# Performance work log

Measured on AMD Instinct MI355X. Metric: run time of the kernel, lower is better.

Reference implementation:

```python
import jax, jax.numpy as jnp
import numpy as np

# Straight-through sign binarization (Binarize in BNN code mutates .data, so
# autograd sees identity -> custom_vjp with identity backward).
@jax.custom_vjp
def binarize(x):
    return jnp.sign(x)

def _bin_fwd(x):
    return jnp.sign(x), None

def _bin_bwd(_, g):
    return (g,)

binarize.defvjp(_bin_fwd, _bin_bwd)

EPS = 1e-5  # torch BatchNorm1d default eps

def batchnorm(x, g, b):
    # training-mode BN: batch statistics, biased variance
    if x.ndim == 3:  # (N, C, L): stats over N and L
        m = x.mean(axis=(0, 2), keepdims=True)
        v = x.var(axis=(0, 2), keepdims=True)
        return (x - m) / jnp.sqrt(v + EPS) * g[None, :, None] + b[None, :, None]
    m = x.mean(axis=0)
    v = x.var(axis=0)
    return (x - m) / jnp.sqrt(v + EPS) * g + b

def hardtanh(x):
    return jnp.clip(x, -1.0, 1.0)

def maxpool3(x):
    # MaxPool1d(kernel=3, stride=3): trim then reshape-max
    N, C, L = x.shape
    Lp = L // 3
    return x[:, :, :Lp * 3].reshape(N, C, Lp, 3).max(axis=-1)

def bconv(x, w, b, binarize_input=True):
    # BinarizeConv1d: kernel 41, dilation 2, VALID padding; weights sign-binarized,
    # inputs binarized except when in_channels == 3 (first layer rule in BNN code).
    xb = binarize(x) if binarize_input else x
    wb = binarize(w)
    y = jax.lax.conv_general_dilated(
        xb, wb, window_strides=(1,), padding='VALID',
        rhs_dilation=(2,), dimension_numbers=('NCH', 'OIH', 'NCH'))
    return y + b[None, :, None]

def blinear(x, w, b):
    # BinarizeLinear: in_features 832/1024 != 784 -> binarize input and weight
    return binarize(x) @ binarize(w).T + b

def _forward(x, bn0_g, bn0_b, conv1_w, conv1_b, bn1_g, bn1_b,
             conv2_w, conv2_b, bn2_g, bn2_b, conv3_w, conv3_b,
             bn3_g, bn3_b, conv4_w, conv4_b, bn4_g, bn4_b,
             conv5_w, conv5_b, fc1_w, fc1_b, bn5_g, bn5_b,
             fc2_w, fc2_b, bn6_g, bn6_b):
    h = hardtanh(batchnorm(x, bn0_g, bn0_b))
    h = maxpool3(bconv(h, conv1_w, conv1_b, binarize_input=False))  # (N,64,5306)
    h = hardtanh(batchnorm(h, bn1_g, bn1_b))
    h = maxpool3(bconv(h, conv2_w, conv2_b))  # (N,64,1742)
    h = hardtanh(batchnorm(h, bn2_g, bn2_b))
    h = maxpool3(bconv(h, conv3_w, conv3_b))  # (N,64,554)
    h = hardtanh(batchnorm(h, bn3_g, bn3_b))
    h = maxpool3(bconv(h, conv4_w, conv4_b))  # (N,64,158)
    h = hardtanh(batchnorm(h, bn4_g, bn4_b))
    h = maxpool3(bconv(h, conv5_w, conv5_b))  # (N,32,26)
    h = h.reshape(-1, 16 * 52)                # (N, 832)
    h = hardtanh(batchnorm(blinear(h, fc1_w, fc1_b), bn5_g, bn5_b))
    h = batchnorm(blinear(h, fc2_w, fc2_b), bn6_g, bn6_b)
    return jax.nn.log_softmax(h, axis=1)

def setup_inputs() -> dict:
    key = jax.random.key(0)
    ks = jax.random.split(key, 32)
    def rn(k, shape, s=0.1):
        return jax.random.normal(k, shape, dtype=jnp.float32) * s
    def bn_params(kg, kb, c):
        return 1.0 + rn(kg, (c,)), rn(kb, (c,))
    N, L, K = 64, 16000, 41
    d = {"x": jax.random.normal(ks[0], (N, 3, L), dtype=jnp.float32)}
    d["bn0_g"], d["bn0_b"] = bn_params(ks[1], ks[2], 3)
    d["conv1_w"], d["conv1_b"] = rn(ks[3], (64, 3, K)), rn(ks[4], (64,), 0.01)
    d["bn1_g"], d["bn1_b"] = bn_params(ks[5], ks[6], 64)
    d["conv2_w"], d["conv2_b"] = rn(ks[7], (64, 64, K)), rn(ks[8], (64,), 0.01)
    d["bn2_g"], d["bn2_b"] = bn_params(ks[9], ks[10], 64)
    d["conv3_w"], d["conv3_b"] = rn(ks[11], (64, 64, K)), rn(ks[12], (64,), 0.01)
    d["bn3_g"], d["bn3_b"] = bn_params(ks[13], ks[14], 64)
    d["conv4_w"], d["conv4_b"] = rn(ks[15], (64, 64, K)), rn(ks[16], (64,), 0.01)
    d["bn4_g"], d["bn4_b"] = bn_params(ks[17], ks[18], 64)
    d["conv5_w"], d["conv5_b"] = rn(ks[19], (32, 64, K)), rn(ks[20], (32,), 0.01)
    d["fc1_w"], d["fc1_b"] = rn(ks[21], (1024, 832)), rn(ks[22], (1024,), 0.01)
    d["bn5_g"], d["bn5_b"] = bn_params(ks[23], ks[24], 1024)
    d["fc2_w"], d["fc2_b"] = rn(ks[25], (1000, 1024)), rn(ks[26], (1000,), 0.01)
    d["bn6_g"], d["bn6_b"] = bn_params(ks[27], ks[28], 1000)
    return d

def reference(x, bn0_g, bn0_b, conv1_w, conv1_b, bn1_g, bn1_b,
              conv2_w, conv2_b, bn2_g, bn2_b, conv3_w, conv3_b,
              bn3_g, bn3_b, conv4_w, conv4_b, bn4_g, bn4_b,
              conv5_w, conv5_b, fc1_w, fc1_b, bn5_g, bn5_b,
              fc2_w, fc2_b, bn6_g, bn6_b):
    return _forward(x, bn0_g, bn0_b, conv1_w, conv1_b, bn1_g, bn1_b,
                    conv2_w, conv2_b, bn2_g, bn2_b, conv3_w, conv3_b,
                    bn3_g, bn3_b, conv4_w, conv4_b, bn4_g, bn4_b,
                    conv5_w, conv5_b, fc1_w, fc1_b, bn5_g, bn5_b,
                    fc2_w, fc2_b, bn6_g, bn6_b)
```

## Files before the change

kernel.cpp:

```cpp
#include <hip/hip_runtime.h>
#include <hip/hip_bf16.h>
#include <stdint.h>

typedef __hip_bfloat16 bf16;
typedef unsigned long long u64;
typedef unsigned short u16;

typedef __attribute__((ext_vector_type(8))) short bf16x8;
typedef __attribute__((ext_vector_type(4))) float f32x4;

#define FIXCAP (1u << 20)

static __device__ __forceinline__ float ldin(const void* p, long i, int f32) {
    return f32 ? ((const float*)p)[i] : __bfloat162float(((const bf16*)p)[i]);
}

__global__ void k_probe(const void* x, unsigned* ctl) {
    int tid = threadIdx.x;
    int good = 0;
    for (int i = tid; i < 1024; i += 256) {
        float v = __bfloat162float(((const bf16*)x)[2 * i]);
        float a = fabsf(v);
        if (v == 0.0f || (isfinite(v) && a >= 1e-4f && a <= 100.0f)) good++;
    }
    __shared__ int s[256];
    s[tid] = good; __syncthreads();
    for (int st = 128; st > 0; st >>= 1) {
        if (tid < st) s[tid] += s[tid + st];
        __syncthreads();
    }
    if (tid == 0) { ctl[0] = 0u; ctl[1] = (s[0] >= 700) ? 0u : 1u; }
}

__global__ void k_sentinel(void* outv, const unsigned* ctl, float val) {
    int i = blockIdx.x * 256 + threadIdx.x;
    if (i >= 64000) return;
    if (ctl[1]) ((float*)outv)[i] = val;
    else ((bf16*)outv)[i] = __float2bfloat16(val);
}

__device__ __forceinline__ void pack_convw_task(const void* w, uint2* wp, int Co, int f32,
                                                int bx, int tid) {
    int t = bx * 256 + tid;
    if (t >= Co * 41) return;
    int co = t / 41, k = t % 41;
    unsigned w0 = 0, w1 = 0;
    for (int c = 0; c < 32; c++)
        if (ldin(w, (co * 64 + c) * 41 + k, f32) > 0.f) w0 |= (1u << c);
    for (int c = 0; c < 32; c++)
        if (ldin(w, (co * 64 + 32 + c) * 41 + k, f32) > 0.f) w1 |= (1u << c);
    wp[t] = make_uint2(w0, w1);
}
__device__ __forceinline__ void pack_rows_task(const void* w, unsigned* wp, int rows, int F,
                                               int f32, int bx, int tid) {
    int Fw = F >> 5;
    int t = bx * 256 + tid;
    if (t >= rows * Fw) return;
    int r = t / Fw, wi = t % Fw;
    unsigned m = 0;
    for (int j = 0; j < 32; j++)
        if (ldin(w, (long)r * F + wi * 32 + j, f32) > 0.f) m |= (1u << j);
    wp[t] = m;
}

__global__ void k_prep(const void* x, const void* c1w, const void* c2w, const void* c3w,
                       const void* c4w, const void* c5w, const void* f1w, const void* f2w,
                       u16* afrag, uint2* w2p, uint2* w3p, uint2* w4p, uint2* w5p,
                       unsigned* fc1wp, unsigned* fc2wp, u64* stats, double* part0,
                       const unsigned* ctl) {
    int f32 = ctl[1];
    int task = blockIdx.y, bx = blockIdx.x, tid = threadIdx.x;
    switch (task) {
        case 0: {
            int t = bx * 256 + tid;
            if (t < 2304) {
                int m = t / 576, rem = t - m * 576;
                int ks = rem / 64, lane = rem - ks * 64;
                int li = lane & 15, hq = lane >> 4;
                int row = 16 * m + li;
                int g = 4 * ks + hq;
                int c = g / 11, t0 = 4 * (g - 11 * c);
                u16* outp = afrag + (size_t)t * 8;
                for (int i2 = 0; i2 < 4; i2++) {
                    int tt = t0 + i2;
                    u16 sv = 0;
                    if (g < 33 && tt <= 40) {
                        float wv = ldin(c1w, (row * 3 + c) * 41 + tt, f32);
                        sv = (wv > 0.f) ? (u16)0x3F80 : ((wv < 0.f) ? (u16)0xBF80 : (u16)0);
                    }
                    outp[2 * i2] = sv;
                    outp[2 * i2 + 1] = sv;
                }
            }
        } break;
        case 1: pack_convw_task(c2w, w2p, 64, f32, bx, tid); break;
        case 2: pack_convw_task(c3w, w3p, 64, f32, bx, tid); break;
        case 3: pack_convw_task(c4w, w4p, 64, f32, bx, tid); break;
        case 4: pack_convw_task(c5w, w5p, 32, f32, bx, tid); break;
        case 5: pack_rows_task(f1w, fc1wp, 1024, 832, f32, bx, tid); break;
        case 6: pack_rows_task(f2w, fc2wp, 1000, 1024, f32, bx, tid); break;
        case 7: {
            int i = bx * 256 + tid;
            if (i < 14400) stats[i] = 0ull;
        } break;
        case 8: {
            if (bx >= 96) return;
            int c = bx >> 5, s = bx & 31;
            double s1 = 0, s2 = 0;
            for (int n = 0; n < 64; n++) {
                long base = (long)(n * 3 + c) * 16000;
                for (int l = s * 256 + tid; l < 16000; l += 32 * 256) {
                    double v = (double)ldin(x, base + l, f32);
                    s1 += v; s2 += v * v;
                }
            }
            __shared__ double a1[256], a2[256];
            a1[tid] = s1; a2[tid] = s2;
            __syncthreads();
            for (int st = 128; st > 0; st >>= 1) {
                if (tid < st) { a1[tid] += a1[tid + st]; a2[tid] += a2[tid + st]; }
                __syncthreads();
            }
            if (tid == 0) { part0[(c * 32 + s) * 2] = a1[0]; part0[(c * 32 + s) * 2 + 1] = a2[0]; }
        } break;
    }
}

__global__ __launch_bounds__(256, 4) void k_conv1(const void* __restrict__ x,
                                                  const double* __restrict__ part0,
                                                  const void* __restrict__ g0,
                                                  const void* __restrict__ b0,
                                                  const u16* __restrict__ afrag,
                                                  double* __restrict__ yb,
                                                  const void* __restrict__ g1,
                                                  const void* __restrict__ b1,
                                                  uint2* __restrict__ x2p,
                                                  unsigned* __restrict__ fixcnt,
                                                  unsigned* __restrict__ fixlist,
                                                  const unsigned* __restrict__ ctl,
                                                  int pass) {
    __shared__ unsigned xs[8][140];
    __shared__ float pool[4][48][20];
    __shared__ double sbuf[4][64][2];
    __shared__ unsigned char sb[4][16][64];
    __shared__ double2 pqs[64];
    __shared__ float2 b0f[3];
    int f32 = ctl[1];
    int n = blockIdx.y, bx = blockIdx.x, tid = threadIdx.x;
    if (tid < 3) {
        int c = tid;
        double s1 = 0, s2 = 0;
        for (int s = 0; s < 32; s++) { s1 += part0[(c * 32 + s) * 2]; s2 += part0[(c * 32 + s) * 2 + 1]; }
        double M = 64.0 * 16000.0;
        double mu = s1 / M, var = s2 / M - mu * mu;
        double A = (double)ldin(g0, c, f32) / sqrt(var + 1e-5);
        b0f[c] = make_float2((float)A, (float)((double)ldin(b0, c, f32) - mu * A));
    }
    if (pass && tid >= 64 && tid < 128) {
        int c = tid - 64;
        double s1 = 0, s2 = 0;
        for (int s = 0; s < 16; s++) { s1 += yb[(c * 16 + s) * 2]; s2 += yb[(c * 16 + s) * 2 + 1]; }
        double M = 64.0 * 5306.0;
        double mu = s1 / M, var = s2 / M - mu * mu;
        double A = (double)ldin(g1, c, f32) / sqrt(var + 1e-5);
        pqs[c] = make_double2(A, (double)ldin(b1, c, f32) - mu * A);
    }
    __syncthreads();

    unsigned* xsf = &xs[0][0];
    for (int f = tid; f < 1120; f += 256) {
        int rc = f / 140, qi = f - rc * 140;
        int r = rc >> 2, c = rc & 3;
        unsigned dw = 0u;
        if (c < 3) {
            int xpos = 192 * bx + 2 * qi + r;
            if (xpos < 16000) {
                float2 pb = b0f[c];
                float v = fmaf(ldin(x, (long)(n * 3 + c) * 16000 + xpos, f32), pb.x, pb.y);
                v = fminf(fmaxf(v, -1.f), 1.f);
                bf16 h = __float2bfloat16(v);
                float hf = __bfloat162float(h);
                bf16 lo = __float2bfloat16(v - hf);
                dw = (unsigned)__bfloat16_as_ushort(h) | ((unsigned)__bfloat16_as_ushort(lo) << 16);
            }
        }
        xsf[f] = dw;
    }
    __syncthreads();

    int lane = tid & 63;
    int li = lane & 15, hq = lane >> 4;
    int w = __builtin_amdgcn_readfirstlane(tid >> 6);

    f32x4 zz = {0.f, 0.f, 0.f, 0.f};
    f32x4 acc[4][3];
#pragma unroll
    for (int m = 0; m < 4; m++)
#pragma unroll
        for (int nf = 0; nf < 3; nf++) acc[m][nf] = zz;

    int boff[3];
#pragma unroll
    for (int nf = 0; nf < 3; nf++) {
        int pl = 48 * w + 16 * nf + li;
        boff[nf] = (pl & 1) * 560 + (pl >> 1);
    }

    const bf16x8* ag = (const bf16x8*)afrag;
#pragma unroll 1
    for (int ks = 0; ks < 9; ks++) {
        int g = 4 * ks + hq;
        int c = g / 11;
        int kb = c * 140 + 4 * (g - 11 * c);
        bf16x8 a0 = ag[(0 * 9 + ks) * 64 + lane];
        bf16x8 a1 = ag[(1 * 9 + ks) * 64 + lane];
        bf16x8 a2 = ag[(2 * 9 + ks) * 64 + lane];
        bf16x8 a3 = ag[(3 * 9 + ks) * 64 + lane];
#pragma unroll
        for (int nf = 0; nf < 3; nf++) {
            const unsigned* bp = xsf + boff[nf] + kb;
            union { int4 i4; bf16x8 v; } u;
            u.i4 = make_int4(bp[0], bp[1], bp[2], bp[3]);
            acc[0][nf] = __builtin_amdgcn_mfma_f32_16x16x32_bf16(a0, u.v, acc[0][nf], 0, 0, 0);
            acc[1][nf] = __builtin_amdgcn_mfma_f32_16x16x32_bf16(a1, u.v, acc[1][nf], 0, 0, 0);
            acc[2][nf] = __builtin_amdgcn_mfma_f32_16x16x32_bf16(a2, u.v, acc[2][nf], 0, 0, 0);
            acc[3][nf] = __builtin_amdgcn_mfma_f32_16x16x32_bf16(a3, u.v, acc[3][nf], 0, 0, 0);
        }
    }

    int lp0 = 64 * bx + 16 * w;
    if (pass == 0) {
#pragma unroll 1
        for (int m = 0; m < 4; m++) {
#pragma unroll
            for (int nf = 0; nf < 3; nf++)
                *(f32x4*)&pool[w][16 * nf + li][4 * hq] = acc[m][nf];
            double s = 0.0, q = 0.0;
#pragma unroll
            for (int i = 0; i < 4; i++) {
                int pc = hq + 4 * i;
                float mq = fmaxf(fmaxf(pool[w][3 * pc][li], pool[w][3 * pc + 1][li]),
                                 pool[w][3 * pc + 2][li]);
                if (lp0 + pc < 5306) {
                    double d = (double)mq;
                    s += d; q += d * d;
                }
            }
            s += __shfl_down(s, 32, 64); s += __shfl_down(s, 16, 64);
            q += __shfl_down(q, 32, 64); q += __shfl_down(q, 16, 64);
            if (lane < 16) { sbuf[w][16 * m + lane][0] = s; sbuf[w][16 * m + lane][1] = q; }
        }
        __syncthreads();
        if (tid < 64) {
            double s = sbuf[0][tid][0] + sbuf[1][tid][0] + sbuf[2][tid][0] + sbuf[3][tid][0];
            double q = sbuf[0][tid][1] + sbuf[1][tid][1] + sbuf[2][tid][1] + sbuf[3][tid][1];
            int sbk = bx & 15;
            atomicAdd(&yb[(tid * 16 + sbk) * 2], s);
            atomicAdd(&yb[(tid * 16 + sbk) * 2 + 1], q);
        }
    } else {
#pragma unroll 1
        for (int m = 0; m < 4; m++) {
#pragma unroll
            for (int nf = 0; nf < 3; nf++)
                *(f32x4*)&pool[w][16 * nf + li][4 * hq] = acc[m][nf];
            int c = 16 * m + li;
            double2 P = pqs[c];
            double athr = 2e-3 * fabs(P.x);
#pragma unroll
            for (int i = 0; i < 4; i++) {
                int pc = hq + 4 * i;
                int lp = lp0 + pc;
                float mq = fmaxf(fmaxf(pool[w][3 * pc][li], pool[w][3 * pc + 1][li]),
                                 pool[w][3 * pc + 2][li]);
                if (lp < 5306) {
                    double v = (double)mq * P.x + P.y;
                    sb[w][pc][c] = (v > 0.0) ? 1 : 0;
                    if (fabs(v) < athr) {
                        unsigned idx = atomicAdd(fixcnt, 1u);
                        if (idx < FIXCAP)
                            fixlist[idx] = ((unsigned)n << 19) | ((unsigned)c << 13) | (unsigned)lp;
                    }
                }
            }
        }
        __syncthreads();
        if (tid < 64) {
            int lp = 64 * bx + tid;
            if (lp < 5306) {
                const unsigned* sp = (const unsigned*)&sb[tid >> 4][tid & 15][0];
                unsigned w0 = 0, w1 = 0;
#pragma unroll
                for (int jw = 0; jw < 8; jw++)
                    w0 |= (((sp[jw] * 0x01020408u) >> 24) & 0xFu) << (4 * jw);
#pragma unroll
                for (int jw = 8; jw < 16; jw++)
                    w1 |= (((sp[jw] * 0x01020408u) >> 24) & 0xFu) << (4 * (jw - 8));
                x2p[(size_t)n * 5306 + lp] = make_uint2(w0, w1);
            }
        }
    }
}

__global__ void k_fix(const unsigned* __restrict__ fixcnt, const unsigned* __restrict__ fixlist,
                      const double* __restrict__ yb, const void* g1, const void* b1,
                      const void* __restrict__ x, const void* __restrict__ c1w,
                      const double* __restrict__ part0, const void* g0, const void* b0,
                      unsigned* __restrict__ x2p, const unsigned* __restrict__ ctl) {
    int f32 = ctl[1];
    unsigned cnt = min(*fixcnt, FIXCAP);
    for (unsigned t = blockIdx.x * 256 + threadIdx.x; t < cnt; t += gridDim.x * 256) {
        unsigned e = fixlist[t];
        int n = e >> 19, c = (e >> 13) & 63, l = e & 8191;
        double s1 = 0, s2 = 0;
        for (int s = 0; s < 16; s++) { s1 += yb[(c * 16 + s) * 2]; s2 += yb[(c * 16 + s) * 2 + 1]; }
        double M = 64.0 * 5306.0;
        double mu = s1 / M, var = s2 / M - mu * mu;
        double A = (double)ldin(g1, c, f32) / sqrt(var + 1e-5);
        double B = (double)ldin(b1, c, f32) - mu * A;
        double best = -1e300;
        for (int r = 0; r < 3; r++) {
            int pp = 3 * l + r;
            double acc = 0.0;
            for (int cc = 0; cc < 3; cc++) {
                double p1 = 0, p2 = 0;
                for (int s = 0; s < 32; s++) { p1 += part0[(cc * 32 + s) * 2]; p2 += part0[(cc * 32 + s) * 2 + 1]; }
                double M0 = 64.0 * 16000.0;
                double mu0 = p1 / M0, var0 = p2 / M0 - mu0 * mu0;
                double A0 = (double)ldin(g0, cc, f32) / sqrt(var0 + 1e-5);
                double B0 = (double)ldin(b0, cc, f32) - mu0 * A0;
                for (int k = 0; k < 41; k++) {
                    float wf = ldin(c1w, (c * 3 + cc) * 41 + k, f32);
                    double sgn = (wf > 0.f) ? 1.0 : ((wf < 0.f) ? -1.0 : 0.0);
                    double xv = (double)ldin(x, (long)(n * 3 + cc) * 16000 + pp + 2 * k, f32);
                    xv = fmin(fmax(xv * A0 + B0, -1.0), 1.0);
                    acc = fma(sgn, xv, acc);
                }
            }
            best = fmax(best, acc);
        }
        double v = best * A + B;
        unsigned* word = &x2p[((size_t)n * 5306 + l) * 2 + (c >> 5)];
        unsigned bit = 1u << (c & 31);
        if (v > 0.0) atomicOr(word, bit);
        else atomicAnd(word, ~bit);
    }
}

__global__ __launch_bounds__(256) void k_conv_bin(const uint2* __restrict__ xp,
                                                  const uint2* __restrict__ wp,
                                                  u16* __restrict__ mout,
                                                  int Lp, int Lin, int Co,
                                                  u64* __restrict__ stat) {
    int n = blockIdx.y, tid = threadIdx.x;
    int lane = tid & 63;
    int wave = __builtin_amdgcn_readfirstlane(tid >> 6);
    int co0 = blockIdx.z * 32 + wave * 8;
    int base = blockIdx.x * 192;
    int lp = blockIdx.x * 64 + lane;

    __shared__ uint2 xt[272];
    for (int i = tid; i < 272; i += 256) {
        int pos = base + i;
        xt[i] = (pos < Lin) ? xp[(size_t)n * Lin + pos] : make_uint2(0u, 0u);
    }
    __syncthreads();

    int acc[8][3] = {};
    uint2 xa = xt[3 * lane];
    for (int k = 0; k < 41; k++) {
        uint2 xb = xt[3 * lane + 2 * k + 1];
        uint2 xc = xt[3 * lane + 2 * k + 2];
#pragma unroll
        for (int j = 0; j < 8; j++) {
            uint2 w = wp[(co0 + j) * 41 + k];
            acc[j][0] += __popc(w.x ^ xa.x) + __popc(w.y ^ xa.y);
            acc[j][1] += __popc(w.x ^ xb.x) + __popc(w.y ^ xb.y);
            acc[j][2] += __popc(w.x ^ xc.x) + __popc(w.y ^ xc.y);
        }
        xa = xc;
    }
    bool ok = lp < Lp;
    int sb = blockIdx.x & 15;
#pragma unroll
    for (int j = 0; j < 8; j++) {
        int m = min(min(acc[j][0], acc[j][1]), acc[j][2]);
        if (ok) mout[((size_t)n * Co + co0 + j) * Lp + lp] = (u16)m;
        unsigned s = ok ? (unsigned)m : 0u;
        unsigned q = ok ? (unsigned)(m * m) : 0u;
        for (int off = 32; off > 0; off >>= 1) {
            s += __shfl_down(s, off, 64);
            q += __shfl_down(q, off, 64);
        }
        if (lane == 0) {
            atomicAdd(&stat[((co0 + j) * 16 + sb) * 2], (u64)s);
            atomicAdd(&stat[((co0 + j) * 16 + sb) * 2 + 1], (u64)q);
        }
    }
}

__global__ __launch_bounds__(256) void k_conv_binm(const u16* __restrict__ min_,
                                                   const u64* __restrict__ statIn,
                                                   const void* g, const void* b, double M,
                                                   const uint2* __restrict__ wp,
                                                   u16* __restrict__ mout,
                                                   u64* __restrict__ statOut,
                                                   int Lp, int Lin, int Co,
                                                   const unsigned* __restrict__ ctl) {
    __shared__ double2 pqs[64];
    __shared__ uint2 xt[272];
    int f32 = ctl[1];
    int n = blockIdx.y, tid = threadIdx.x;
    if (tid < 64) {
        int c = tid;
        u64 s1 = 0, s2 = 0;
        for (int s = 0; s < 16; s++) { s1 += statIn[(c * 16 + s) * 2]; s2 += statIn[(c * 16 + s) * 2 + 1]; }
        double mu = (double)s1 / M;
        double varm = (double)s2 / M - mu * mu;
        double A = (double)ldin(g, c, f32) / sqrt(4.0 * varm + 1e-5);
        pqs[c] = make_double2(-2.0 * A, 2.0 * A * mu + (double)ldin(b, c, f32));
    }
    __syncthreads();
    int base = blockIdx.x * 192;
    for (int i = tid; i < 272; i += 256) {
        int pos = base + i;
        unsigned w0 = 0, w1 = 0;
        if (pos < Lin) {
            const u16* mp = min_ + (size_t)n * 64 * Lin + pos;
#pragma unroll 4
            for (int c = 0; c < 32; c++) {
                double2 p = pqs[c];
                if ((double)mp[(size_t)c * Lin] * p.x + p.y > 0.0) w0 |= 1u << c;
            }
#pragma unroll 4
            for (int c = 0; c < 32; c++) {
                double2 p = pqs[c + 32];
                if ((double)mp[(size_t)(c + 32) * Lin] * p.x + p.y > 0.0) w1 |= 1u << c;
            }
        }
        xt[i] = make_uint2(w0, w1);
    }
    __syncthreads();

    int lane = tid & 63;
    int wave = __builtin_amdgcn_readfirstlane(tid >> 6);
    int co0 = blockIdx.z * 32 + wave * 8;
    int lp = blockIdx.x * 64 + lane;

    int acc[8][3] = {};
    uint2 xa = xt[3 * lane];
    for (int k = 0; k < 41; k++) {
        uint2 xb = xt[3 * lane + 2 * k + 1];
        uint2 xc = xt[3 * lane + 2 * k + 2];
#pragma unroll
        for (int j = 0; j < 8; j++) {
            uint2 w = wp[(co0 + j) * 41 + k];
            acc[j][0] += __popc(w.x ^ xa.x) + __popc(w.y ^ xa.y);
            acc[j][1] += __popc(w.x ^ xb.x) + __popc(w.y ^ xb.y);
            acc[j][2] += __popc(w.x ^ xc.x) + __popc(w.y ^ xc.y);
        }
        xa = xc;
    }
    bool ok = lp < Lp;
    int sb = blockIdx.x & 15;
#pragma unroll
    for (int j = 0; j < 8; j++) {
        int m = min(min(acc[j][0], acc[j][1]), acc[j][2]);
        if (ok) mout[((size_t)n * Co + co0 + j) * Lp + lp] = (u16)m;
        if (statOut) {
            unsigned s = ok ? (unsigned)m : 0u;
            unsigned q = ok ? (unsigned)(m * m) : 0u;
            for (int off = 32; off > 0; off >>= 1) {
                s += __shfl_down(s, off, 64);
                q += __shfl_down(q, off, 64);
            }
            if (lane == 0) {
                atomicAdd(&statOut[((co0 + j) * 16 + sb) * 2], (u64)s);
                atomicAdd(&statOut[((co0 + j) * 16 + sb) * 2 + 1], (u64)q);
            }
        }
    }
}

__global__ void k_c5fc1(const u16* __restrict__ m4, const u64* __restrict__ s4,
                        const void* g4, const void* b4,
                        const uint2* __restrict__ w5p, const void* __restrict__ b5,
                        const unsigned* __restrict__ fc1wp, u16* __restrict__ acc1,
                        u64* __restrict__ s5, const unsigned* __restrict__ ctl) {
    __shared__ double2 pqs[64];
    __shared__ uint2 xt[280];
    __shared__ int m5s[32][26];
    __shared__ unsigned xw[26];
    int f32 = ctl[1];
    int n = blockIdx.x, tid = threadIdx.x;
    const int Lin = 158;
    if (tid < 64) {
        int c = tid;
        u64 s1 = 0, s2 = 0;
        for (int s = 0; s < 16; s++) { s1 += s4[(c * 16 + s) * 2]; s2 += s4[(c * 16 + s) * 2 + 1]; }
        double M = 64.0 * 158.0;
        double mu = (double)s1 / M;
        double varm = (double)s2 / M - mu * mu;
        double A = (double)ldin(g4, c, f32) / sqrt(4.0 * varm + 1e-5);
        pqs[c] = make_double2(-2.0 * A, 2.0 * A * mu + (double)ldin(b4, c, f32));
    }
    __syncthreads();
    for (int i = tid; i < 280; i += 256) {
        unsigned w0 = 0, w1 = 0;
        if (i < Lin) {
            const u16* mp = m4 + (size_t)n * 64 * Lin + i;
#pragma unroll 4
            for (int c = 0; c < 32; c++) {
                double2 p = pqs[c];
                if ((double)mp[(size_t)c * Lin] * p.x + p.y > 0.0) w0 |= 1u << c;
            }
#pragma unroll 4
            for (int c = 0; c < 32; c++) {
                double2 p = pqs[c + 32];
                if ((double)mp[(size_t)(c + 32) * Lin] * p.x + p.y > 0.0) w1 |= 1u << c;
            }
        }
        xt[i] = make_uint2(w0, w1);
    }
    __syncthreads();

    int lane = tid & 63;
    int wave = __builtin_amdgcn_readfirstlane(tid >> 6);
    int co0 = wave * 8;
    int acc[8][3] = {};
    uint2 xa = xt[3 * lane];
    for (int k = 0; k < 41; k++) {
        uint2 xb = xt[3 * lane + 2 * k + 1];
        uint2 xc = xt[3 * lane + 2 * k + 2];
#pragma unroll
        for (int j = 0; j < 8; j++) {
            uint2 w = w5p[(co0 + j) * 41 + k];
            acc[j][0] += __popc(w.x ^ xa.x) + __popc(w.y ^ xa.y);
            acc[j][1] += __popc(w.x ^ xb.x) + __popc(w.y ^ xb.y);
            acc[j][2] += __popc(w.x ^ xc.x) + __popc(w.y ^ xc.y);
        }
        xa = xc;
    }
    if (lane < 26) {
#pragma unroll
        for (int j = 0; j < 8; j++)
            m5s[co0 + j][lane] = min(min(acc[j][0], acc[j][1]), acc[j][2]);
    }
    __syncthreads();
    if (tid < 26) {
        unsigned mask = 0;
        for (int j = 0; j < 32; j++) {
            int f = tid * 32 + j, c = f / 26, l = f % 26;
            double yv = 2624.0 - 2.0 * (double)m5s[c][l] + (double)ldin(b5, c, f32);
            if (yv > 0.0) mask |= 1u << j;
        }
        xw[tid] = mask;
    }
    __syncthreads();
#pragma unroll
    for (int i = 0; i < 4; i++) {
        int j = tid + i * 256;
        unsigned a = 0;
        for (int w = 0; w < 26; w++) a += __popc(xw[w] ^ fc1wp[j * 26 + w]);
        acc1[n * 1024 + j] = (u16)a;
        atomicAdd(&s5[j * 2], (u64)a);
        atomicAdd(&s5[j * 2 + 1], (u64)(a * a));
    }
}

__global__ void k_fc2(const u16* __restrict__ acc1, const u64* __restrict__ s5,
                      const void* g5, const void* b5, const unsigned* __restrict__ fc2wp,
                      u16* __restrict__ acc2, u64* __restrict__ s6, const unsigned* ctl) {
    __shared__ double2 pq5s[1024];
    __shared__ unsigned xw[32];
    int f32 = ctl[1];
    int n = blockIdx.y, tid = threadIdx.x;
    for (int f = tid; f < 1024; f += 256) {
        u64 a1 = s5[f * 2], a2 = s5[f * 2 + 1];
        double mu = (double)a1 / 64.0;
        double varm = (double)a2 / 64.0 - mu * mu;
        double A = (double)ldin(g5, f, f32) / sqrt(4.0 * varm + 1e-5);
        pq5s[f] = make_double2(-2.0 * A, 2.0 * A * mu + (double)ldin(b5, f, f32));
    }
    __syncthreads();
    if (tid < 32) {
        unsigned mask = 0;
        for (int j = 0; j < 32; j++) {
            int f = tid * 32 + j;
            double2 p = pq5s[f];
            if ((double)acc1[n * 1024 + f] * p.x + p.y > 0.0) mask |= 1u << j;
        }
        xw[tid] = mask;
    }
    __syncthreads();
    int j = blockIdx.x * 256 + tid;
    if (j >= 1000) return;
    unsigned a = 0;
    for (int w = 0; w < 32; w++) a += __popc(xw[w] ^ fc2wp[j * 32 + w]);
    acc2[n * 1000 + j] = (u16)a;
    atomicAdd(&s6[j * 2], (u64)a);
    atomicAdd(&s6[j * 2 + 1], (u64)(a * a));
}

__global__ void k_lsm(const u16* __restrict__ acc2, const u64* __restrict__ s6,
                      const void* g6, const void* b6, const unsigned* ctl, void* outv) {
    int n = blockIdx.x, tid = threadIdx.x;
    int f32 = ctl[1];
    __shared__ double red[256];
    double v[4];
    double mx = -1e300;
#pragma unroll
    for (int i = 0; i < 4; i++) {
        int j = tid + i * 256;
        if (j < 1000) {
            u64 a1 = s6[j * 2], a2 = s6[j * 2 + 1];
            double mu = (double)a1 / 64.0;
            double varm = (double)a2 / 64.0 - mu * mu;
            double A = (double)ldin(g6, j, f32) / sqrt(4.0 * varm + 1e-5);
            v[i] = (double)acc2[n * 1000 + j] * (-2.0 * A) + (2.0 * A * mu + (double)ldin(b6, j, f32));
            mx = fmax(mx, v[i]);
        } else v[i] = -1e300;
    }
    red[tid] = mx; __syncthreads();
    for (int s = 128; s > 0; s >>= 1) {
        if (tid < s) red[tid] = fmax(red[tid], red[tid + s]);
        __syncthreads();
    }
    mx = red[0]; __syncthreads();
    double sum = 0.0;
#pragma unroll
    for (int i = 0; i < 4; i++) {
        int j = tid + i * 256;
        if (j < 1000) sum += exp(v[i] - mx);
    }
    red[tid] = sum; __syncthreads();
    for (int s = 128; s > 0; s >>= 1) {
        if (tid < s) red[tid] += red[tid + s];
        __syncthreads();
    }
    double ls = log(red[0]);
#pragma unroll
    for (int i = 0; i < 4; i++) {
        int j = tid + i * 256;
        if (j < 1000) {
            float r = (float)(v[i] - mx - ls);
            if (!isfinite(r)) r = -700.0f;
            if (f32) ((float*)outv)[n * 1000 + j] = r;
            else ((bf16*)outv)[n * 1000 + j] = __float2bfloat16(r);
        }
    }
}

extern "C" void kernel_launch(void* const* d_in, const int* in_sizes, int n_in,
                              void* d_out, int out_size, void* d_ws, size_t ws_size,
                              hipStream_t stream) {
    const void* x       = d_in[0];
    const void* bn0_g   = d_in[1];
    const void* bn0_b   = d_in[2];
    const void* conv1_w = d_in[3];
    const void* bn1_g   = d_in[5];
    const void* bn1_b   = d_in[6];
    const void* conv2_w = d_in[7];
    const void* bn2_g   = d_in[9];
    const void* bn2_b   = d_in[10];
    const void* conv3_w = d_in[11];
    const void* bn3_g   = d_in[13];
    const void* bn3_b   = d_in[14];
    const void* conv4_w = d_in[15];
    const void* bn4_g   = d_in[17];
    const void* bn4_b   = d_in[18];
    const void* conv5_w = d_in[19];
    const void* conv5_b = d_in[20];
    const void* fc1_w   = d_in[21];
    const void* bn5_g   = d_in[23];
    const void* bn5_b   = d_in[24];
    const void* fc2_w   = d_in[25];
    const void* bn6_g   = d_in[27];
    const void* bn6_b   = d_in[28];

    char* wsb = (char*)d_ws;
    size_t off = 0;
    auto alloc = [&](size_t bytes) -> void* {
        off = (off + 255) & ~(size_t)255;
        void* p = wsb + off;
        off += bytes;
        return p;
    };

    unsigned* ctl   = (unsigned*)alloc(256);
    unsigned* x2p   = (unsigned*)alloc(2716672);
    u16*      m2    = (u16*)alloc(14270464);
    u16*      m3    = (u16*)alloc(4538368);
    u16*      m4    = (u16*)alloc(1294336);
    u16*      acc1  = (u16*)alloc(131072);
    u16*      acc2  = (u16*)alloc(128000);
    u16*      afrag = (u16*)alloc(36864);
    uint2*    w2p   = (uint2*)alloc(20992);
    uint2*    w3p   = (uint2*)alloc(20992);
    uint2*    w4p   = (uint2*)alloc(20992);
    uint2*    w5p   = (uint2*)alloc(10496);
    unsigned* fc1wp = (unsigned*)alloc(106496);
    unsigned* fc2wp = (unsigned*)alloc(128000);
    u64*      stats = (u64*)alloc(14400 * 8);
    double*   part0 = (double*)alloc(2048);
    unsigned* fixlist = (unsigned*)alloc(FIXCAP * 4);
    size_t need = (off + 255) & ~(size_t)255;

    u64* s2 = stats;
    u64* s3 = stats + 2048;
    u64* s4 = stats + 4096;
    u64* s5 = stats + 6144;
    u64* s6 = stats + 8192;
    double* yb = (double*)(stats + 12288);
    unsigned* fixcnt = (unsigned*)(stats + 14340);

    k_probe<<<1, 256, 0, stream>>>(x, ctl);

    if (n_in != 29) {
        k_sentinel<<<250, 256, 0, stream>>>(d_out, ctl, -(3000.0f + (float)n_in));
        return;
    }
    if (ws_size < need) {
        k_sentinel<<<250, 256, 0, stream>>>(d_out, ctl, -1500.0f);
        return;
    }

    k_prep<<<dim3(125, 9), 256, 0, stream>>>(x, conv1_w, conv2_w, conv3_w, conv4_w, conv5_w,
                                             fc1_w, fc2_w, afrag, w2p, w3p, w4p, w5p,
                                             fc1wp, fc2wp, stats, part0, ctl);

    k_conv1<<<dim3(83, 64), 256, 0, stream>>>(x, part0, bn0_g, bn0_b, afrag, yb,
                                              bn1_g, bn1_b, (uint2*)x2p,
                                              fixcnt, fixlist, ctl, 0);
    k_conv1<<<dim3(83, 64), 256, 0, stream>>>(x, part0, bn0_g, bn0_b, afrag, yb,
                                              bn1_g, bn1_b, (uint2*)x2p,
                                              fixcnt, fixlist, ctl, 1);
    k_fix<<<64, 256, 0, stream>>>(fixcnt, fixlist, yb, bn1_g, bn1_b, x, conv1_w,
                                  part0, bn0_g, bn0_b, x2p, ctl);

    k_conv_bin<<<dim3(28, 64, 2), 256, 0, stream>>>((const uint2*)x2p, w2p, m2, 1742, 5306, 64, s2);
    k_conv_binm<<<dim3(9, 64, 2), 256, 0, stream>>>(m2, s2, bn2_g, bn2_b, 64.0 * 1742.0,
                                                    w3p, m3, s3, 554, 1742, 64, ctl);
    k_conv_binm<<<dim3(3, 64, 2), 256, 0, stream>>>(m3, s3, bn3_g, bn3_b, 64.0 * 554.0,
                                                    w4p, m4, s4, 158, 554, 64, ctl);

    k_c5fc1<<<64, 256, 0, stream>>>(m4, s4, bn4_g, bn4_b, w5p, conv5_b, fc1wp, acc1, s5, ctl);
    k_fc2<<<dim3(4, 64), 256, 0, stream>>>(acc1, s5, bn5_g, bn5_b, fc2wp, acc2, s6, ctl);
    k_lsm<<<64, 256, 0, stream>>>(acc2, s6, bn6_g, bn6_b, ctl, d_out);
}
```

Measured before the change: 806.4 us.

## Replace popcount conv2 with int8 MFMA convolution over ±1 expanded bits

Conv2 (64→64 channels, binarized) was computed with XOR-popcount on packed bits. It now expands the packed input bits to ±1 int8 in LDS and pre-packs weights as ±1 int8 MFMA fragments. The convolution then runs on mfma_i32_16x16x64_i8 matrix instructions, with weight chunks streamed via global_load_lds. Pooling and stats are done through an LDS staging buffer, and the dot product is converted back to the mismatch count. The aim is to move the heavy popcount ALU work onto matrix cores, at the cost of more LDS traffic and an 8x larger input footprint.

Measured after the change: 883.1 us. +9.5%, slower.

```diff
diff --git a/kernel.cpp b/kernel.cpp
--- a/kernel.cpp
+++ b/kernel.cpp
@@ -8,6 +8,7 @@
 
 typedef __attribute__((ext_vector_type(8))) short bf16x8;
 typedef __attribute__((ext_vector_type(4))) float f32x4;
+typedef __attribute__((ext_vector_type(4))) int i32x4;
 
 #define FIXCAP (1u << 20)
 
@@ -65,7 +66,7 @@
 
 __global__ void k_prep(const void* x, const void* c1w, const void* c2w, const void* c3w,
                        const void* c4w, const void* c5w, const void* f1w, const void* f2w,
-                       u16* afrag, uint2* w2p, uint2* w3p, uint2* w4p, uint2* w5p,
+                       u16* afrag, signed char* af2, uint2* w3p, uint2* w4p, uint2* w5p,
                        unsigned* fc1wp, unsigned* fc2wp, u64* stats, double* part0,
                        const unsigned* ctl) {
     int f32 = ctl[1];
@@ -93,7 +94,31 @@
                 }
             }
         } break;
-        case 1: pack_convw_task(c2w, w2p, 64, f32, bx, tid); break;
+        case 1: {
+            int t = bx * 256 + tid;
+            if (t < 11264) {
+                int lane = t & 63, g = t >> 6;
+                int m = g & 3, tt = g >> 2;
+                int li = lane & 15, hq = lane >> 4;
+                int co = 16 * m + li;
+                unsigned dws[4];
+#pragma unroll
+                for (int dw = 0; dw < 4; dw++) {
+                    unsigned v = 0;
+                    if (tt <= 40) {
+#pragma unroll
+                        for (int b = 0; b < 4; b++) {
+                            int c = 16 * hq + 4 * dw + b;
+                            float wv = ldin(c2w, (co * 64 + c) * 41 + tt, f32);
+                            unsigned byte = (wv > 0.f) ? 0x01u : 0xFFu;
+                            v |= byte << (8 * b);
+                        }
+                    }
+                    dws[dw] = v;
+                }
+                ((uint4*)af2)[t] = make_uint4(dws[0], dws[1], dws[2], dws[3]);
+            }
+        } break;
         case 2: pack_convw_task(c3w, w3p, 64, f32, bx, tid); break;
         case 3: pack_convw_task(c4w, w4p, 64, f32, bx, tid); break;
         case 4: pack_convw_task(c5w, w5p, 32, f32, bx, tid); break;
@@ -347,54 +372,113 @@
     }
 }
 
-__global__ __launch_bounds__(256) void k_conv_bin(const uint2* __restrict__ xp,
-                                                  const uint2* __restrict__ wp,
-                                                  u16* __restrict__ mout,
-                                                  int Lp, int Lin, int Co,
-                                                  u64* __restrict__ stat) {
-    int n = blockIdx.y, tid = threadIdx.x;
+__global__ __launch_bounds__(256, 3) void k_conv_i8(const uint2* __restrict__ xp,
+                                                    const signed char* __restrict__ af2,
+                                                    u16* __restrict__ mout,
+                                                    u64* __restrict__ stat) {
+    __shared__ unsigned xsd[2 * 136 * 16];
+    __shared__ __align__(16) signed char abuf[16384];
+    __shared__ int pooli[4][48][20];
+    int n = blockIdx.y, bx = blockIdx.x, tid = threadIdx.x;
+    int base = 192 * bx;
+
+    for (int e = tid; e < 272; e += 256) {
+        int pos = base + e;
+        int r = e & 1, qi = e >> 1;
+        unsigned* dst = xsd + (r * 136 + qi) * 16;
+        if (pos < 5306) {
+            uint2 mk = xp[(size_t)n * 5306 + pos];
+#pragma unroll
+            for (int dw = 0; dw < 8; dw++) {
+                unsigned nib = (mk.x >> (4 * dw)) & 0xFu;
+                unsigned sp = (nib * 0x00204081u) & 0x01010101u;
+                dst[dw] = ~(sp * 0xFEu);
+            }
+#pragma unroll
+            for (int dw = 0; dw < 8; dw++) {
+                unsigned nib = (mk.y >> (4 * dw)) & 0xFu;
+                unsigned sp = (nib * 0x00204081u) & 0x01010101u;
+                dst[8 + dw] = ~(sp * 0xFEu);
+            }
+        } else {
+#pragma unroll
+            for (int dw = 0; dw < 16; dw++) dst[dw] = 0u;
+        }
+    }
+
     int lane = tid & 63;
-    int wave = __builtin_amdgcn_readfirstlane(tid >> 6);
-    int co0 = blockIdx.z * 32 + wave * 8;
-    int base = blockIdx.x * 192;
-    int lp = blockIdx.x * 64 + lane;
-
-    __shared__ uint2 xt[272];
-    for (int i = tid; i < 272; i += 256) {
-        int pos = base + i;
-        xt[i] = (pos < Lin) ? xp[(size_t)n * Lin + pos] : make_uint2(0u, 0u);
-    }
-    __syncthreads();
-
-    int acc[8][3] = {};
-    uint2 xa = xt[3 * lane];
-    for (int k = 0; k < 41; k++) {
-        uint2 xb = xt[3 * lane + 2 * k + 1];
-        uint2 xc = xt[3 * lane + 2 * k + 2];
-#pragma unroll
-        for (int j = 0; j < 8; j++) {
-            uint2 w = wp[(co0 + j) * 41 + k];
-            acc[j][0] += __popc(w.x ^ xa.x) + __popc(w.y ^ xa.y);
-            acc[j][1] += __popc(w.x ^ xb.x) + __popc(w.y ^ xb.y);
-            acc[j][2] += __popc(w.x ^ xc.x) + __popc(w.y ^ xc.y);
-        }
-        xa = xc;
-    }
-    bool ok = lp < Lp;
-    int sb = blockIdx.x & 15;
-#pragma unroll
-    for (int j = 0; j < 8; j++) {
-        int m = min(min(acc[j][0], acc[j][1]), acc[j][2]);
-        if (ok) mout[((size_t)n * Co + co0 + j) * Lp + lp] = (u16)m;
-        unsigned s = ok ? (unsigned)m : 0u;
-        unsigned q = ok ? (unsigned)(m * m) : 0u;
-        for (int off = 32; off > 0; off >>= 1) {
-            s += __shfl_down(s, off, 64);
-            q += __shfl_down(q, off, 64);
-        }
-        if (lane == 0) {
-            atomicAdd(&stat[((co0 + j) * 16 + sb) * 2], (u64)s);
-            atomicAdd(&stat[((co0 + j) * 16 + sb) * 2 + 1], (u64)q);
+    int li = lane & 15, hq = lane >> 4;
+    int w = __builtin_amdgcn_readfirstlane(tid >> 6);
+
+    i32x4 zz = {0, 0, 0, 0};
+    i32x4 acc[4][3];
+#pragma unroll
+    for (int m = 0; m < 4; m++)
+#pragma unroll
+        for (int nf = 0; nf < 3; nf++) acc[m][nf] = zz;
+
+    int boff[3];
+#pragma unroll
+    for (int nf = 0; nf < 3; nf++) {
+        int pl = 48 * w + 16 * nf + li;
+        boff[nf] = ((pl & 1) * 136 + (pl >> 1)) * 64 + 16 * hq;
+    }
+
+    const char* gA = (const char*)af2 + w * 4096 + lane * 16;
+    const char* xsb = (const char*)xsd;
+
+#pragma unroll 1
+    for (int ch = 0; ch < 11; ch++) {
+        __syncthreads();
+#pragma unroll
+        for (int k2 = 0; k2 < 4; k2++)
+            __builtin_amdgcn_global_load_lds((const uint4*)(gA + ch * 16384 + k2 * 1024),
+                                             (uint4*)&abuf[w * 4096 + k2 * 1024], 16, 0, 0);
+        __syncthreads();
+#pragma unroll
+        for (int tl = 0; tl < 4; tl++) {
+            int t = 4 * ch + tl;
+            i32x4 a0 = *(const i32x4*)&abuf[((tl * 4 + 0) * 64 + lane) * 16];
+            i32x4 a1 = *(const i32x4*)&abuf[((tl * 4 + 1) * 64 + lane) * 16];
+            i32x4 a2 = *(const i32x4*)&abuf[((tl * 4 + 2) * 64 + lane) * 16];
+            i32x4 a3 = *(const i32x4*)&abuf[((tl * 4 + 3) * 64 + lane) * 16];
+#pragma unroll
+            for (int nf = 0; nf < 3; nf++) {
+                i32x4 b = *(const i32x4*)(xsb + boff[nf] + t * 64);
+                acc[0][nf] = __builtin_amdgcn_mfma_i32_16x16x64_i8(a0, b, acc[0][nf], 0, 0, 0);
+                acc[1][nf] = __builtin_amdgcn_mfma_i32_16x16x64_i8(a1, b, acc[1][nf], 0, 0, 0);
+                acc[2][nf] = __builtin_amdgcn_mfma_i32_16x16x64_i8(a2, b, acc[2][nf], 0, 0, 0);
+                acc[3][nf] = __builtin_amdgcn_mfma_i32_16x16x64_i8(a3, b, acc[3][nf], 0, 0, 0);
+            }
+        }
+    }
+
+    int sbk = bx & 15;
+#pragma unroll 1
+    for (int m = 0; m < 4; m++) {
+#pragma unroll
+        for (int nf = 0; nf < 3; nf++)
+            *(i32x4*)&pooli[w][16 * nf + li][4 * hq] = acc[m][nf];
+        int c = 16 * m + li;
+        unsigned s = 0, q = 0;
+#pragma unroll
+        for (int i = 0; i < 4; i++) {
+            int pc = hq + 4 * i;
+            int d = max(max(pooli[w][3 * pc][li], pooli[w][3 * pc + 1][li]),
+                        pooli[w][3 * pc + 2][li]);
+            int mv = (2624 - d) >> 1;
+            int lp = 64 * bx + 16 * w + pc;
+            if (lp < 1742) {
+                mout[((size_t)n * 64 + c) * 1742 + lp] = (u16)mv;
+                s += (unsigned)mv;
+                q += (unsigned)(mv * mv);
+            }
+        }
+        s += __shfl_down(s, 32, 64); s += __shfl_down(s, 16, 64);
+        q += __shfl_down(q, 32, 64); q += __shfl_down(q, 16, 64);
+        if (lane < 16) {
+            atomicAdd(&stat[((16 * m + lane) * 16 + sbk) * 2], (u64)s);
+            atomicAdd(&stat[((16 * m + lane) * 16 + sbk) * 2 + 1], (u64)q);
         }
     }
 }
@@ -466,7 +550,7 @@
 #pragma unroll
     for (int j = 0; j < 8; j++) {
         int m = min(min(acc[j][0], acc[j][1]), acc[j][2]);
-        if (ok) mout[((size_t)n * Co + co0 + j) * Lp + lp] = (u16)m;
+        if (ok) mout[((size_t)n * 64 + co0 + j) * Lp + lp] = (u16)m;
         if (statOut) {
             unsigned s = ok ? (unsigned)m : 0u;
             unsigned q = ok ? (unsigned)(m * m) : 0u;
@@ -695,7 +779,7 @@
     u16*      acc1  = (u16*)alloc(131072);
     u16*      acc2  = (u16*)alloc(128000);
     u16*      afrag = (u16*)alloc(36864);
-    uint2*    w2p   = (uint2*)alloc(20992);
+    signed char* af2 = (signed char*)alloc(180224);
     uint2*    w3p   = (uint2*)alloc(20992);
     uint2*    w4p   = (uint2*)alloc(20992);
     uint2*    w5p   = (uint2*)alloc(10496);
@@ -726,7 +810,7 @@
     }
 
     k_prep<<<dim3(125, 9), 256, 0, stream>>>(x, conv1_w, conv2_w, conv3_w, conv4_w, conv5_w,
-                                             fc1_w, fc2_w, afrag, w2p, w3p, w4p, w5p,
+                                             fc1_w, fc2_w, afrag, af2, w3p, w4p, w5p,
                                              fc1wp, fc2wp, stats, part0, ctl);
 
     k_conv1<<<dim3(83, 64), 256, 0, stream>>>(x, part0, bn0_g, bn0_b, afrag, yb,
@@ -738,7 +822,7 @@
     k_fix<<<64, 256, 0, stream>>>(fixcnt, fixlist, yb, bn1_g, bn1_b, x, conv1_w,
                                   part0, bn0_g, bn0_b, x2p, ctl);
 
-    k_conv_bin<<<dim3(28, 64, 2), 256, 0, stream>>>((const uint2*)x2p, w2p, m2, 1742, 5306, 64, s2);
+    k_conv_i8<<<dim3(28, 64), 256, 0, stream>>>((const uint2*)x2p, af2, m2, s2);
     k_conv_binm<<<dim3(9, 64, 2), 256, 0, stream>>>(m2, s2, bn2_g, bn2_b, 64.0 * 1742.0,
                                                     w3p, m3, s3, 554, 1742, 64, ctl);
     k_conv_binm<<<dim3(3, 64, 2), 256, 0, stream>>>(m3, s3, bn3_g, bn3_b, 64.0 * 554.0,
```
